# Kernel tuning notes

Measured on AMD Instinct MI355X. Metric: run time of the kernel, lower is better.

## Reference

```python
import jax, jax.numpy as jnp
import numpy as np

L, B, D, H = 128, 4, 768, 300
NT, NR = 7, 12  # ner tags, relation types
EPS = 1e-5


def _cummax(v):
    # torch: cumsum(softmax(v, -1), -1)
    return jnp.cumsum(jax.nn.softmax(v, axis=-1), axis=-1)


def _layernorm(v, g, b):
    mu = jnp.mean(v, axis=-1, keepdims=True)
    var = jnp.var(v, axis=-1, keepdims=True)
    return (v - mu) * jax.lax.rsqrt(var + EPS) * g + b


def setup_inputs() -> dict:
    key = jax.random.key(0)
    ks = jax.random.split(key, 24)
    s = lambda fan_in: 1.0 / np.sqrt(fan_in)
    u = lambda k, shape, sc: jax.random.uniform(k, shape, jnp.float32, -sc, sc)
    inp = {
        "x": jax.random.normal(ks[0], (L, B, D), jnp.float32),
        "mask": jnp.ones((L, B), jnp.float32),
        # PFN_Unit
        "W_ih": u(ks[1], (5 * H, D), s(D)), "b_ih": u(ks[2], (5 * H,), s(D)),
        "W_hh": u(ks[3], (5 * H, H), s(H)), "b_hh": u(ks[4], (5 * H,), s(H)),
        "W_tr": u(ks[5], (H, 3 * H), s(3 * H)), "b_tr": u(ks[6], (H,), s(3 * H)),
        # NERUnit
        "n_W": u(ks[7], (H, 2 * H), s(2 * H)), "n_b": u(ks[8], (H,), s(2 * H)),
        "ner_hW": u(ks[9], (H, 3 * H), s(3 * H)), "ner_hb": u(ks[10], (H,), s(3 * H)),
        "ner_g": jnp.ones((H,), jnp.float32), "ner_beta": jnp.zeros((H,), jnp.float32),
        "ner_tW": u(ks[11], (NT, H), s(H)), "ner_tb": u(ks[12], (NT,), s(H)),
        # ReUnit
        "r_W": u(ks[13], (H, 2 * H), s(2 * H)), "r_b": u(ks[14], (H,), s(2 * H)),
        "re_hW": u(ks[15], (H, 3 * H), s(3 * H)), "re_hb": u(ks[16], (H,), s(3 * H)),
        "re_g": jnp.ones((H,), jnp.float32), "re_beta": jnp.zeros((H,), jnp.float32),
        "re_tW": u(ks[17], (NR, H), s(H)), "re_tb": u(ks[18], (NR,), s(H)),
    }
    return inp


def _encoder(x, W_ih, b_ih, W_hh, b_hh, W_tr, b_tr):
    pre = jnp.einsum('lbd,gd->lbg', x, W_ih) + b_ih  # precompute input transform [L,B,5H]

    def step(carry, gx):
        h, c_in = carry
        gates = gx + h @ W_hh.T + b_hh
        c, eg_cin, rg_cin, eg_c, rg_c = jnp.split(gates, 5, axis=1)
        eg_cin, rg_cin = 1.0 - _cummax(eg_cin), _cummax(rg_cin)
        eg_c, rg_c = 1.0 - _cummax(eg_c), _cummax(rg_c)
        c = jnp.tanh(c)
        ov_c = rg_c * eg_c
        up_c, dn_c = rg_c - ov_c, eg_c - ov_c
        ov_i = rg_cin * eg_cin
        up_i, dn_i = rg_cin - ov_i, eg_cin - ov_i
        share = ov_i * c_in + ov_c * c
        c_re = up_i * c_in + up_c * c + share
        c_ner = dn_i * c_in + dn_c * c + share
        c_out = jnp.concatenate([c_re, c_ner, share], axis=-1) @ W_tr.T + b_tr
        h_out = jnp.tanh(c_out)
        return (h_out, c_out), (jnp.tanh(c_ner), jnp.tanh(c_re), jnp.tanh(share))

    h0 = jnp.zeros((x.shape[1], W_hh.shape[1]), x.dtype)
    _, (h_ner, h_re, h_share) = jax.lax.scan(step, (h0, h0), pre)
    return h_ner, h_re, h_share  # each [L,B,H]


def _pair_unit(h_task, h_share, mask, gW, gb, hW, hb, ln_g, ln_b, tW, tb, diag):
    length = h_task.shape[0]
    # global feature: tanh(Linear(cat(share, task))), max over time
    h_glob = jnp.tanh(jnp.concatenate([h_share, h_task], axis=-1) @ gW.T + gb)  # [L,B,H]
    g = jnp.max(h_glob, axis=0)  # [B,H]
    # pairwise feature [L,L,B,3H] = cat(start, end, global)
    st = jnp.broadcast_to(h_task[:, None], (length, length) + h_task.shape[1:])
    en = jnp.broadcast_to(h_task[None, :], (length, length) + h_task.shape[1:])
    gb4 = jnp.broadcast_to(g, (length, length) + g.shape)
    feat = jnp.concatenate([st, en, gb4], axis=-1)
    out = _layernorm(feat @ hW.T + hb, ln_g, ln_b)
    out = jax.nn.elu(out)  # eval mode: dropout is identity
    out = jax.nn.sigmoid(out @ tW.T + tb)  # [L,L,B,T]
    # mask
    m = mask[:, None, :] * mask[None, :, :]  # [L,L,B]
    if diag:
        m = m * jnp.triu(jnp.ones((length, length), out.dtype))[:, :, None]
    return out * m[..., None]


def reference(x, mask, W_ih, b_ih, W_hh, b_hh, W_tr, b_tr,
              n_W, n_b, ner_hW, ner_hb, ner_g, ner_beta, ner_tW, ner_tb,
              r_W, r_b, re_hW, re_hb, re_g, re_beta, re_tW, re_tb):
    h_ner, h_re, h_share = _encoder(x, W_ih, b_ih, W_hh, b_hh, W_tr, b_tr)
    ner = _pair_unit(h_ner, h_share, mask, n_W, n_b, ner_hW, ner_hb,
                     ner_g, ner_beta, ner_tW, ner_tb, diag=True)
    re = _pair_unit(h_re, h_share, mask, r_W, r_b, re_hW, re_hb,
                    re_g, re_beta, re_tW, re_tb, diag=False)
    return ner, re
```

## Files before the change

kernel.cpp:

```cpp
#include <hip/hip_runtime.h>

#define LLEN 128
#define BB 4
#define DD 768
#define HH 300
#define G5 1500
#define H3 900
#define NTT 7
#define NRR 12
#define NCHB 10
#define RPB 150
#define OPB 30

#define C_WIH  0
#define C_X    1152000
#define C_WHH2 1545216
#define C_WTR2 1995216
#define F_BIH  2265216
#define F_BTR  2266720
#define F_PRE  2267040
#define F_HG0  (F_PRE)
#define F_HG1  (F_PRE+153600)
#define F_A0   (F_PRE+307200)
#define F_E0   (F_PRE+460800)
#define F_GF0  (F_PRE+616832)
#define F_GF1  (F_PRE+618048)
#define F_HNER (F_PRE+768000)
#define F_HRE  (F_HNER+153600)
#define F_HSH  (F_HRE+153600)
#define F_A1   0
#define F_E1   153600
#define F_AUX  (F_HSH+153600)
#define AUXB   2432
#define AUX_FL 9728
#define WS_NEED_BYTES ((size_t)(F_AUX+10752)*4)

typedef unsigned short u16;
typedef unsigned int u32;

__device__ __forceinline__ float bf2f(u16 u) {
  union { u32 i; float f; } v; v.i = ((u32)u) << 16; return v.f;
}
__device__ __forceinline__ u16 f2bf(float f) {
  union { float f; u32 i; } v; v.f = f;
  u32 r = v.i + 0x7fffu + ((v.i >> 16) & 1u);
  return (u16)(r >> 16);
}
__device__ __forceinline__ float ldin(const void* p, int i, bool f32) {
  return f32 ? ((const float*)p)[i] : bf2f(((const u16*)p)[i]);
}
__device__ __forceinline__ bool is32(const void* mk) {
  return ((const u16*)mk)[0] == 0;
}
__device__ __forceinline__ float wsum(float x) {
  #pragma unroll
  for (int d = 1; d < 64; d <<= 1) x += __shfl_xor(x, d);
  return x;
}
__device__ __forceinline__ float aload(const float* p) {
  int v = __hip_atomic_load((const int*)p, __ATOMIC_RELAXED, __HIP_MEMORY_SCOPE_AGENT);
  union { int i; float f; } u; u.i = v; return u.f;
}
__device__ __forceinline__ void astore(float* p, float v) {
  union { float f; int i; } u; u.f = v;
  __hip_atomic_store((int*)p, u.i, __ATOMIC_RELAXED, __HIP_MEMORY_SCOPE_AGENT);
}
__device__ __forceinline__ void gbar(int* flag, int tid, int target) {
  __syncthreads();
  if (tid == 0) {
    __builtin_amdgcn_s_waitcnt(0);
    __hip_atomic_fetch_add(flag, 1, __ATOMIC_RELAXED, __HIP_MEMORY_SCOPE_AGENT);
    while (__hip_atomic_load(flag, __ATOMIC_RELAXED, __HIP_MEMORY_SCOPE_AGENT) < target)
      __builtin_amdgcn_s_sleep(1);
  }
  __syncthreads();
}

__global__ void k_canon(const void* xo, const void* mk, const void* Wih, const void* bih,
                        const void* Whh, const void* bhh, const void* Wtr, const void* btr,
                        float* ws) {
  bool f32 = is32(mk);
  int piece = blockIdx.y;
  int i = blockIdx.x * 256 + threadIdx.x;
  switch (piece) {
    case 0: if (!f32 && i < 1152000) ws[C_WIH + i] = ldin(Wih, i, f32); break;
    case 1: if (!f32 && i < 393216)  ws[C_X + i]   = ldin(xo, i, f32);  break;
    case 2: if (i < 225000) {
      int k2 = i / G5, out = i - k2 * G5;
      float2 v;
      v.x = ldin(Whh, out * HH + 2 * k2, f32);
      v.y = ldin(Whh, out * HH + 2 * k2 + 1, f32);
      ((float2*)(ws + C_WHH2))[i] = v;
    } break;
    case 3: if (i < 135000) {
      int k2 = i / HH, out = i - k2 * HH;
      float2 v;
      v.x = ldin(Wtr, out * H3 + 2 * k2, f32);
      v.y = ldin(Wtr, out * H3 + 2 * k2 + 1, f32);
      ((float2*)(ws + C_WTR2))[i] = v;
    } break;
    case 4: {
      if (i < 1504) ws[F_BIH + i] = (i < G5) ? ldin(bih, i, f32) + ldin(bhh, i, f32) : 0.f;
      else if (i < 1824) { int j = i - 1504; ws[F_BTR + j] = (j < HH) ? ldin(btr, j, f32) : 0.f; }
    } break;
    case 5: if (i < 1024) ((int*)(ws + F_AUX + AUX_FL))[i] = 0; break;
  }
}

__global__ void k_pre2(const void* xo, const void* Wo, const void* mk,
                       const float* cX, const float* cW, const float* biasf, float* pre) {
  bool f32 = is32(mk);
  const float* X = f32 ? (const float*)xo : cX;
  const float* W = f32 ? (const float*)Wo : cW;
  __shared__ __align__(16) float xl[8 * DD];
  int tid = threadIdx.x;
  int lb0 = (blockIdx.x >> 1) * 8;
  int half = blockIdx.x & 1;
  for (int e = tid; e < 8 * DD; e += 256) xl[e] = X[(size_t)lb0 * DD + e];
  __syncthreads();
  for (int j = half * 750 + tid; j < half * 750 + 750; j += 256) {
    const float4* w = (const float4*)(W + (size_t)j * DD);
    float acc[8] = {0.f, 0.f, 0.f, 0.f, 0.f, 0.f, 0.f, 0.f};
    #pragma unroll 2
    for (int k = 0; k < DD / 4; ++k) {
      float4 u = w[k];
      #pragma unroll
      for (int r = 0; r < 8; ++r) {
        const float4 p = *(const float4*)(xl + r * DD + k * 4);
        acc[r] += u.x * p.x + u.y * p.y + u.z * p.z + u.w * p.w;
      }
    }
    float bias = biasf[j];
    #pragma unroll
    for (int r = 0; r < 8; ++r) pre[(size_t)(lb0 + r) * G5 + j] = acc[r] + bias;
  }
}

__global__ void __launch_bounds__(512, 2) k_scan4(const float* pre, const float2* W2h, const float2* W2t,
                                                  const float* btrf, float* hner, float* hre, float* hsh,
                                                  float* aux) {
  __shared__ __align__(16) float h_l[304];
  __shared__ __align__(16) float ci_l[304];
  __shared__ __align__(16) float ga_l[1504];
  __shared__ __align__(16) float cat_l[904];
  __shared__ __align__(16) float ps[512];
  __shared__ float exv[160];
  __shared__ float pp[40];
  __shared__ float sums_l[8];
  int b = blockIdx.x / NCHB, ch = blockIdx.x % NCHB;
  int s = ch >> 1;
  int r0 = ch * RPB;
  int tid = threadIdx.x;
  float* gb   = aux + b * AUXB;
  float* cb   = gb + 1504;
  float* hb   = gb + 1808;
  float* sums = gb + 2112;
  int* flags = (int*)(aux + AUX_FL) + b * 256;
  for (int i = tid; i < 304; i += 512) { h_l[i] = 0.f; ci_l[i] = 0.f; }
  __syncthreads();
  int j = tid / RPB, r = tid - j * RPB;
  int o2 = tid % OPB, jj = tid / OPB;
  int kb = j * 100;

  float2 wh[50];
  if (tid < 450) {
    const float2* wp = W2h + (size_t)(j * 50) * G5 + (r0 + r);
    #pragma unroll
    for (int kk = 0; kk < 50; ++kk) wh[kk] = wp[(size_t)kk * G5];
  }
  float2 wt[29];
  int k2b = jj * 29;
  int k2e = (k2b + 29 < 450) ? (k2b + 29) : 450;
  int nk2 = k2e - k2b;
  if (tid < 480) {
    const float2* wp = W2t + (size_t)k2b * HH + (ch * OPB + o2);
    #pragma unroll
    for (int q = 0; q < 29; ++q) if (q < nk2) wt[q] = wp[(size_t)q * HH];
  }

  for (int t = 0; t < LLEN; ++t) {
    if (t > 0) {
      for (int i = tid; i < HH; i += 512) { h_l[i] = aload(hb + i); ci_l[i] = aload(cb + i); }
      __syncthreads();
    }
    if (tid < 450) {
      float acc = (j == 0) ? pre[((size_t)t * BB + b) * G5 + r0 + r] : 0.f;
      if (t > 0) {
        #pragma unroll
        for (int kk = 0; kk < 50; ++kk)
          acc += wh[kk].x * h_l[kb + 2 * kk] + wh[kk].y * h_l[kb + 2 * kk + 1];
      }
      ps[tid] = acc;
    }
    __syncthreads();
    if (tid < RPB) {
      float g = ps[tid] + ps[RPB + tid] + ps[2 * RPB + tid];
      if (s == 0) astore(gb + r0 + tid, tanhf(g));
      else exv[tid] = __expf(g);
    }
    __syncthreads();
    if (s > 0) {
      if (tid < 30) {
        int base = tid * 5;
        pp[tid] = ((exv[base] + exv[base+1]) + (exv[base+2] + exv[base+3])) + exv[base+4];
      }
      __syncthreads();
      if (tid == 0) {
        float run = 0.f;
        for (int i = 0; i < 30; ++i) { float tv = pp[i]; pp[i] = run; run += tv; }
        astore(sums + (ch - 2), run);
      }
      __syncthreads();
      if (tid < 30) {
        int base = tid * 5;
        float run = pp[tid];
        run += exv[base];     astore(gb + r0 + base,     run);
        run += exv[base + 1]; astore(gb + r0 + base + 1, run);
        run += exv[base + 2]; astore(gb + r0 + base + 2, run);
        run += exv[base + 3]; astore(gb + r0 + base + 3, run);
        run += exv[base + 4]; astore(gb + r0 + base + 4, run);
      }
    }
    gbar(flags + 2 * t, tid, NCHB);
    for (int i = tid; i < G5; i += 512) ga_l[i] = aload(gb + i);
    if (tid < 8) sums_l[tid] = aload(sums + tid);
    __syncthreads();
    if (tid < HH) {
      float c = ga_l[tid];
      float v[4];
      #pragma unroll
      for (int s1 = 0; s1 < 4; ++s1) {
        float raw = ga_l[(s1 + 1) * HH + tid];
        float off = (tid >= RPB) ? sums_l[2 * s1] : 0.f;
        float S = sums_l[2 * s1] + sums_l[2 * s1 + 1];
        v[s1] = (raw + off) / S;
      }
      float eg_cin = 1.f - v[0], rg_cin = v[1], eg_c = 1.f - v[2], rg_c = v[3];
      float ci = (t > 0) ? ci_l[tid] : 0.f;
      float ov_c = rg_c * eg_c;
      float up_c = rg_c - ov_c, dn_c = eg_c - ov_c;
      float ov_i = rg_cin * eg_cin;
      float up_i = rg_cin - ov_i, dn_i = eg_cin - ov_i;
      float share = ov_i * ci + ov_c * c;
      float c_re  = up_i * ci + up_c * c + share;
      float c_ner = dn_i * ci + dn_c * c + share;
      cat_l[tid] = c_re; cat_l[HH + tid] = c_ner; cat_l[2 * HH + tid] = share;
      int sb = ch * OPB;
      if (tid >= sb && tid < sb + OPB) {
        size_t ob = ((size_t)t * BB + b) * HH + tid;
        hner[ob] = tanhf(c_ner); hre[ob] = tanhf(c_re); hsh[ob] = tanhf(share);
      }
    }
    __syncthreads();
    if (tid < 480) {
      float acc = 0.f;
      #pragma unroll
      for (int q = 0; q < 29; ++q)
        if (q < nk2) acc += wt[q].x * cat_l[2 * (k2b + q)] + wt[q].y * cat_l[2 * (k2b + q) + 1];
      ps[tid] = acc;
    }
    __syncthreads();
    if (tid < OPB) {
      float co = btrf[ch * OPB + tid];
      #pragma unroll
      for (int q = 0; q < 16; ++q) co += ps[q * OPB + tid];
      astore(cb + ch * OPB + tid, co);
      astore(hb + ch * OPB + tid, tanhf(co));
    }
    gbar(flags + 2 * t + 1, tid, NCHB);
  }
}

__global__ void k_glob3(const float* hsh, const float* hner, const float* hre,
                        const void* nW, const void* nb, const void* rW, const void* rb,
                        const void* mk, float* hg0, float* hg1) {
  bool f32 = is32(mk);
  int task = blockIdx.x >> 7;
  int lb0 = (blockIdx.x & 127) * 4;
  const float* tsk = task ? hre : hner;
  const void* gWo = task ? rW : nW;
  const void* gbo = task ? rb : nb;
  float* hg = task ? hg1 : hg0;
  __shared__ __align__(16) float catl[2400];
  int tid = threadIdx.x;
  for (int e = tid; e < 2400; e += 320) {
    int rr = e / 600, c = e - rr * 600;
    catl[e] = (c < HH) ? hsh[(size_t)(lb0 + rr) * HH + c] : tsk[(size_t)(lb0 + rr) * HH + (c - HH)];
  }
  __syncthreads();
  if (tid < HH) {
    float bias = ldin(gbo, tid, f32);
    float acc[4] = {bias, bias, bias, bias};
    if (f32) {
      const float4* row = (const float4*)((const float*)gWo + (size_t)tid * 600);
      #pragma unroll 2
      for (int k = 0; k < 150; ++k) {
        float4 u = row[k];
        #pragma unroll
        for (int rr = 0; rr < 4; ++rr) {
          const float4 cv = *(const float4*)(catl + rr * 600 + 4 * k);
          acc[rr] += u.x * cv.x + u.y * cv.y + u.z * cv.z + u.w * cv.w;
        }
      }
    } else {
      for (int k = 0; k < 600; ++k) {
        float w = ldin(gWo, tid * 600 + k, f32);
        #pragma unroll
        for (int rr = 0; rr < 4; ++rr) acc[rr] += w * catl[rr * 600 + k];
      }
    }
    #pragma unroll
    for (int rr = 0; rr < 4; ++rr) hg[(size_t)(lb0 + rr) * HH + tid] = tanhf(acc[rr]);
  }
}

__global__ void k_feat2(const float* hner, const float* hre,
                        const void* nhW, const void* nhb, const void* rhW, const void* rhb,
                        const void* mk, float* A0, float* E0, float* A1, float* E1) {
  bool f32 = is32(mk);
  int task = blockIdx.x >> 7;
  int lb0 = (blockIdx.x & 127) * 4;
  const float* tsk = task ? hre : hner;
  const void* hWo = task ? rhW : nhW;
  const void* hbo = task ? rhb : nhb;
  float* A = task ? A1 : A0;
  float* E = task ? E1 : E0;
  __shared__ __align__(16) float tl[1200];
  int tid = threadIdx.x;
  for (int e = tid; e < 1200; e += 320) {
    int rr = e / 300, c = e - rr * 300;
    tl[e] = tsk[(size_t)(lb0 + rr) * HH + c];
  }
  __syncthreads();
  if (tid < HH) {
    float bias = ldin(hbo, tid, f32);
    float a[4] = {bias, bias, bias, bias};
    float ev[4] = {0.f, 0.f, 0.f, 0.f};
    if (f32) {
      const float4* r1 = (const float4*)((const float*)hWo + (size_t)tid * H3);
      const float4* r2 = (const float4*)((const float*)hWo + (size_t)tid * H3 + HH);
      #pragma unroll 2
      for (int k = 0; k < 75; ++k) {
        float4 u = r1[k], w2 = r2[k];
        #pragma unroll
        for (int rr = 0; rr < 4; ++rr) {
          const float4 tv = *(const float4*)(tl + rr * 300 + 4 * k);
          a[rr]  += u.x * tv.x + u.y * tv.y + u.z * tv.z + u.w * tv.w;
          ev[rr] += w2.x * tv.x + w2.y * tv.y + w2.z * tv.z + w2.w * tv.w;
        }
      }
    } else {
      for (int k = 0; k < HH; ++k) {
        float w1 = ldin(hWo, tid * H3 + k, f32);
        float w2 = ldin(hWo, tid * H3 + HH + k, f32);
        #pragma unroll
        for (int rr = 0; rr < 4; ++rr) {
          a[rr] += w1 * tl[rr * 300 + k];
          ev[rr] += w2 * tl[rr * 300 + k];
        }
      }
    }
    #pragma unroll
    for (int rr = 0; rr < 4; ++rr) {
      A[(size_t)(lb0 + rr) * HH + tid] = a[rr];
      E[(size_t)(lb0 + rr) * HH + tid] = ev[rr];
    }
  }
}

__global__ void k_gmf(const float* hg0, const float* hg1, const void* nhW, const void* rhW,
                      const void* mk, float* Gf0, float* Gf1) {
  bool f32 = is32(mk);
  int task = blockIdx.x >> 2, b = blockIdx.x & 3;
  const float* hg = task ? hg1 : hg0;
  const void* hWo = task ? rhW : nhW;
  float* Gf = task ? Gf1 : Gf0;
  __shared__ __align__(16) float gl[304];
  int tid = threadIdx.x;
  if (tid < HH) {
    float m = -1e30f;
    for (int l = 0; l < LLEN; ++l) m = fmaxf(m, hg[((size_t)l * BB + b) * HH + tid]);
    gl[tid] = m;
  }
  __syncthreads();
  if (tid < HH) {
    float acc = 0.f;
    if (f32) {
      const float4* row = (const float4*)((const float*)hWo + (size_t)tid * H3 + 600);
      #pragma unroll 5
      for (int k = 0; k < 75; ++k) {
        float4 u = row[k];
        const float4 gv = *(const float4*)(gl + 4 * k);
        acc += u.x * gv.x + u.y * gv.y + u.z * gv.z + u.w * gv.w;
      }
    } else {
      for (int k = 0; k < HH; ++k) acc += gl[k] * ldin(hWo, tid * H3 + 600 + k, f32);
    }
    Gf[b * HH + tid] = acc;
  }
}

__global__ void __launch_bounds__(256) k_pair6(const float* A0, const float* E0, const float* Gf0,
                                               const void* lg0, const void* lb0_, const void* tW0, const void* tb0,
                                               const float* A1, const float* E1, const float* Gf1,
                                               const void* lg1, const void* lb1_, const void* tW1, const void* tb1,
                                               const void* mk, void* outv) {
  __shared__ float lg_l[304], lb_l[304], tb_l[16];
  __shared__ float tw_l[3616];
  bool f32 = is32(mk);
  int tau = blockIdx.x >> 12;
  int bid = blockIdx.x & 4095;
  const float* A  = tau ? A1 : A0;
  const float* E  = tau ? E1 : E0;
  const float* Gf = tau ? Gf1 : Gf0;
  const void* lgo = tau ? lg1 : lg0;
  const void* lbo = tau ? lb1_ : lb0_;
  const void* tWo = tau ? tW1 : tW0;
  const void* tbo = tau ? tb1 : tb0;
  int T = tau ? NRR : NTT;
  int diag = tau ? 0 : 1;
  int Toff = tau ? 458752 : 0;
  int tid = threadIdx.x;
  for (int i2 = tid; i2 < HH; i2 += 256) { lg_l[i2] = ldin(lgo, i2, f32); lb_l[i2] = ldin(lbo, i2, f32); }
  for (int i2 = tid; i2 < T * HH; i2 += 256) tw_l[i2] = ldin(tWo, i2, f32);
  if (tid < T) tb_l[tid] = ldin(tbo, tid, f32);
  __syncthreads();
  int i = bid >> 5;
  int j0 = (bid & 31) << 2;
  int b = tid >> 6, ln = tid & 63;
  const float* ar = A  + (size_t)(i * BB + b) * HH;
  const float* gr = Gf + (size_t)b * HH;
  bool ok4 = ln < 44;
  float a0 = ar[ln]       + gr[ln];
  float a1 = ar[64 + ln]  + gr[64 + ln];
  float a2 = ar[128 + ln] + gr[128 + ln];
  float a3 = ar[192 + ln] + gr[192 + ln];
  float a4 = ok4 ? (ar[256 + ln] + gr[256 + ln]) : 0.f;
  float mi = ldin(mk, i * BB + b, f32);
  for (int dj = 0; dj < 4; ++dj) {
    int jx = j0 + dj;
    const float* er = E + (size_t)(jx * BB + b) * HH;
    float u0 = a0 + er[ln];
    float u1 = a1 + er[64 + ln];
    float u2 = a2 + er[128 + ln];
    float u3 = a3 + er[192 + ln];
    float u4 = ok4 ? (a4 + er[256 + ln]) : 0.f;
    float s1 = ((u0 + u1) + (u2 + u3)) + u4;
    float s2 = ((u0 * u0 + u1 * u1) + (u2 * u2 + u3 * u3)) + u4 * u4;
    #pragma unroll
    for (int d = 1; d < 64; d <<= 1) { s1 += __shfl_xor(s1, d); s2 += __shfl_xor(s2, d); }
    float mean = s1 * (1.f / 300.f);
    float var = s2 * (1.f / 300.f) - mean * mean;
    float rstd = rsqrtf(var + 1e-5f);
    {
      float y;
      y = (u0 - mean) * rstd * lg_l[ln]       + lb_l[ln];       u0 = (y > 0.f) ? y : __expf(y) - 1.f;
      y = (u1 - mean) * rstd * lg_l[64 + ln]  + lb_l[64 + ln];  u1 = (y > 0.f) ? y : __expf(y) - 1.f;
      y = (u2 - mean) * rstd * lg_l[128 + ln] + lb_l[128 + ln]; u2 = (y > 0.f) ? y : __expf(y) - 1.f;
      y = (u3 - mean) * rstd * lg_l[192 + ln] + lb_l[192 + ln]; u3 = (y > 0.f) ? y : __expf(y) - 1.f;
      if (ok4) {
        y = (u4 - mean) * rstd * lg_l[256 + ln] + lb_l[256 + ln];
        u4 = (y > 0.f) ? y : __expf(y) - 1.f;
      }
    }
    float m = mi * ldin(mk, jx * BB + b, f32);
    if (diag && jx < i) m = 0.f;
    size_t obase = (size_t)Toff + ((size_t)(i * LLEN + jx) * BB + b) * T;
    float mine = 0.f;
    for (int t = 0; t < T; ++t) {
      const float* twr = tw_l + t * HH;
      float s = u0 * twr[ln] + u1 * twr[64 + ln] + u2 * twr[128 + ln] + u3 * twr[192 + ln];
      if (ok4) s += u4 * twr[256 + ln];
      s = wsum(s);
      s += tb_l[t];
      float o = m / (1.f + __expf(-s));
      mine = (ln == t) ? o : mine;
    }
    if (ln < T) {
      if (f32) ((float*)outv)[obase + ln] = mine;
      else ((u16*)outv)[obase + ln] = f2bf(mine);
    }
  }
}

__global__ void k_sent(const void* mk, const void* xo, void* outv, int hostcode) {
  __shared__ int bad;
  if (threadIdx.x == 0) bad = 0;
  __syncthreads();
  bool f32 = is32(mk);
  for (int i = threadIdx.x; i < 4096; i += 256) {
    float v = ldin(xo, i, f32);
    if (!(v == v) || fabsf(v) > 1e6f) bad = 1;
  }
  __syncthreads();
  if (threadIdx.x == 0) {
    float code = (float)hostcode;
    if (bad) code = fmaxf(code, 88.f);
    if (code > 0.f) {
      if (f32) ((float*)outv)[0] = code;
      else ((u16*)outv)[0] = f2bf(code);
    }
  }
}

extern "C" void kernel_launch(void* const* d_in, const int* in_sizes, int n_in,
                              void* d_out, int out_size, void* d_ws, size_t ws_size,
                              hipStream_t stream) {
  const void* x    = d_in[0];
  const void* mask = d_in[1];
  const void* Wih  = d_in[2];
  const void* bih  = d_in[3];
  const void* Whh  = d_in[4];
  const void* bhh  = d_in[5];
  const void* Wtr  = d_in[6];
  const void* btr  = d_in[7];
  const void* nW   = d_in[8];
  const void* nb   = d_in[9];
  const void* nhW  = d_in[10];
  const void* nhb  = d_in[11];
  const void* ng   = d_in[12];
  const void* nbe  = d_in[13];
  const void* ntW  = d_in[14];
  const void* ntb  = d_in[15];
  const void* rW   = d_in[16];
  const void* rb   = d_in[17];
  const void* rhW  = d_in[18];
  const void* rhb  = d_in[19];
  const void* rg   = d_in[20];
  const void* rbe  = d_in[21];
  const void* rtW  = d_in[22];
  const void* rtb  = d_in[23];
  float* ws = (float*)d_ws;

  static const int exp_sz[24] = {393216, 512, 1152000, 1500, 450000, 1500, 270000, 300,
                                 180000, 300, 270000, 300, 300, 300, 2100, 7,
                                 180000, 300, 270000, 300, 300, 300, 3600, 12};
  int hostcode = 0;
  if (n_in != 24) hostcode = 890;
  else {
    for (int ii = 0; ii < 24; ++ii)
      if (in_sizes[ii] != exp_sz[ii]) { hostcode = 900 + ii; break; }
  }
  if (hostcode == 0 && out_size != 1245184) hostcode = 880;
  if (hostcode == 0 && ws_size < WS_NEED_BYTES) hostcode = 1099;

  dim3 gc(4500, 6);
  k_canon<<<gc, 256, 0, stream>>>(x, mask, Wih, bih, Whh, bhh, Wtr, btr, ws);
  k_pre2<<<128, 256, 0, stream>>>(x, Wih, mask, ws + C_X, ws + C_WIH, ws + F_BIH, ws + F_PRE);
  k_scan4<<<40, 512, 0, stream>>>(ws + F_PRE, (const float2*)(ws + C_WHH2), (const float2*)(ws + C_WTR2),
                                  ws + F_BTR, ws + F_HNER, ws + F_HRE, ws + F_HSH, ws + F_AUX);
  k_glob3<<<256, 320, 0, stream>>>(ws + F_HSH, ws + F_HNER, ws + F_HRE,
                                   nW, nb, rW, rb, mask, ws + F_HG0, ws + F_HG1);
  k_feat2<<<256, 320, 0, stream>>>(ws + F_HNER, ws + F_HRE, nhW, nhb, rhW, rhb, mask,
                                   ws + F_A0, ws + F_E0, ws + F_A1, ws + F_E1);
  k_gmf<<<8, 320, 0, stream>>>(ws + F_HG0, ws + F_HG1, nhW, rhW, mask, ws + F_GF0, ws + F_GF1);
  k_pair6<<<8192, 256, 0, stream>>>(ws + F_A0, ws + F_E0, ws + F_GF0, ng, nbe, ntW, ntb,
                                    ws + F_A1, ws + F_E1, ws + F_GF1, rg, rbe, rtW, rtb,
                                    mask, d_out);
  k_sent<<<1, 256, 0, stream>>>(mask, x, d_out, hostcode);
}
```

Measured before the change: 1.544 ms.

## Drop weight transposes, fuse glob/feat kernels, widen pair tiles, warp-scan prefix

The scan kernel now reads W_hh and W_tr straight from the original inputs in row-major form instead of from pre-transposed workspace copies, so the canon kernel no longer transposes them. Canon is split into a bf16-only conversion kernel that exits early for fp32 inputs plus a small kernel for biases and flag clearing. The glob and feat kernels are merged into one launch, and the pair kernel gives each block 8 columns instead of 4, halving its grid. The serial 30-element prefix sum in the scan is replaced by a shuffle-based wave scan. Per-thread weight loads in the scan become strided in a different pattern, which may change how coalesced they are.

```diff
diff --git a/kernel.cpp b/kernel.cpp
--- a/kernel.cpp
+++ b/kernel.cpp
@@ -14,8 +14,6 @@
 
 #define C_WIH  0
 #define C_X    1152000
-#define C_WHH2 1545216
-#define C_WTR2 1995216
 #define F_BIH  2265216
 #define F_BTR  2266720
 #define F_PRE  2267040
@@ -76,35 +74,20 @@
   __syncthreads();
 }
 
-__global__ void k_canon(const void* xo, const void* mk, const void* Wih, const void* bih,
-                        const void* Whh, const void* bhh, const void* Wtr, const void* btr,
-                        float* ws) {
-  bool f32 = is32(mk);
+__global__ void k_canon2(const void* xo, const void* mk, const void* Wih, float* ws) {
+  if (is32(mk)) return;
   int piece = blockIdx.y;
   int i = blockIdx.x * 256 + threadIdx.x;
-  switch (piece) {
-    case 0: if (!f32 && i < 1152000) ws[C_WIH + i] = ldin(Wih, i, f32); break;
-    case 1: if (!f32 && i < 393216)  ws[C_X + i]   = ldin(xo, i, f32);  break;
-    case 2: if (i < 225000) {
-      int k2 = i / G5, out = i - k2 * G5;
-      float2 v;
-      v.x = ldin(Whh, out * HH + 2 * k2, f32);
-      v.y = ldin(Whh, out * HH + 2 * k2 + 1, f32);
-      ((float2*)(ws + C_WHH2))[i] = v;
-    } break;
-    case 3: if (i < 135000) {
-      int k2 = i / HH, out = i - k2 * HH;
-      float2 v;
-      v.x = ldin(Wtr, out * H3 + 2 * k2, f32);
-      v.y = ldin(Wtr, out * H3 + 2 * k2 + 1, f32);
-      ((float2*)(ws + C_WTR2))[i] = v;
-    } break;
-    case 4: {
-      if (i < 1504) ws[F_BIH + i] = (i < G5) ? ldin(bih, i, f32) + ldin(bhh, i, f32) : 0.f;
-      else if (i < 1824) { int j = i - 1504; ws[F_BTR + j] = (j < HH) ? ldin(btr, j, f32) : 0.f; }
-    } break;
-    case 5: if (i < 1024) ((int*)(ws + F_AUX + AUX_FL))[i] = 0; break;
-  }
+  if (piece == 0) { if (i < 1152000) ws[C_WIH + i] = bf2f(((const u16*)Wih)[i]); }
+  else            { if (i < 393216)  ws[C_X + i]   = bf2f(((const u16*)xo)[i]); }
+}
+
+__global__ void k_misc(const void* bih, const void* bhh, const void* btr, const void* mk, float* ws) {
+  bool f32 = is32(mk);
+  int i = blockIdx.x * 256 + threadIdx.x;
+  if (i < 1504) ws[F_BIH + i] = (i < G5) ? ldin(bih, i, f32) + ldin(bhh, i, f32) : 0.f;
+  else if (i < 1824) { int j = i - 1504; ws[F_BTR + j] = (j < HH) ? ldin(btr, j, f32) : 0.f; }
+  else if (i >= 2048 && i < 3072) ((int*)(ws + F_AUX + AUX_FL))[i - 2048] = 0;
 }
 
 __global__ void k_pre2(const void* xo, const void* Wo, const void* mk,
@@ -136,9 +119,9 @@
   }
 }
 
-__global__ void __launch_bounds__(512, 2) k_scan4(const float* pre, const float2* W2h, const float2* W2t,
-                                                  const float* btrf, float* hner, float* hre, float* hsh,
-                                                  float* aux) {
+__global__ void __launch_bounds__(512, 2) k_scan5(const float* pre, const void* Whh, const void* Wtr,
+                                                  const void* mk, const float* btrf,
+                                                  float* hner, float* hre, float* hsh, float* aux) {
   __shared__ __align__(16) float h_l[304];
   __shared__ __align__(16) float ci_l[304];
   __shared__ __align__(16) float ga_l[1504];
@@ -147,6 +130,7 @@
   __shared__ float exv[160];
   __shared__ float pp[40];
   __shared__ float sums_l[8];
+  bool f32 = is32(mk);
   int b = blockIdx.x / NCHB, ch = blockIdx.x % NCHB;
   int s = ch >> 1;
   int r0 = ch * RPB;
@@ -164,18 +148,31 @@
 
   float2 wh[50];
   if (tid < 450) {
-    const float2* wp = W2h + (size_t)(j * 50) * G5 + (r0 + r);
-    #pragma unroll
-    for (int kk = 0; kk < 50; ++kk) wh[kk] = wp[(size_t)kk * G5];
+    if (f32) {
+      const float2* wp = (const float2*)((const float*)Whh + (size_t)(r0 + r) * HH + kb);
+      #pragma unroll
+      for (int kk = 0; kk < 50; ++kk) wh[kk] = wp[kk];
+    } else {
+      const u16* wp = (const u16*)Whh + (size_t)(r0 + r) * HH + kb;
+      #pragma unroll
+      for (int kk = 0; kk < 50; ++kk) { wh[kk].x = bf2f(wp[2 * kk]); wh[kk].y = bf2f(wp[2 * kk + 1]); }
+    }
   }
   float2 wt[29];
   int k2b = jj * 29;
   int k2e = (k2b + 29 < 450) ? (k2b + 29) : 450;
   int nk2 = k2e - k2b;
   if (tid < 480) {
-    const float2* wp = W2t + (size_t)k2b * HH + (ch * OPB + o2);
-    #pragma unroll
-    for (int q = 0; q < 29; ++q) if (q < nk2) wt[q] = wp[(size_t)q * HH];
+    int out = ch * OPB + o2;
+    if (f32) {
+      const float2* wp = (const float2*)((const float*)Wtr + (size_t)out * H3 + 2 * k2b);
+      #pragma unroll
+      for (int q = 0; q < 29; ++q) if (q < nk2) wt[q] = wp[q];
+    } else {
+      const u16* wp = (const u16*)Wtr + (size_t)out * H3 + 2 * k2b;
+      #pragma unroll
+      for (int q = 0; q < 29; ++q) if (q < nk2) { wt[q].x = bf2f(wp[2 * q]); wt[q].y = bf2f(wp[2 * q + 1]); }
+    }
   }
 
   for (int t = 0; t < LLEN; ++t) {
@@ -205,10 +202,13 @@
         pp[tid] = ((exv[base] + exv[base+1]) + (exv[base+2] + exv[base+3])) + exv[base+4];
       }
       __syncthreads();
-      if (tid == 0) {
-        float run = 0.f;
-        for (int i = 0; i < 30; ++i) { float tv = pp[i]; pp[i] = run; run += tv; }
-        astore(sums + (ch - 2), run);
+      if (tid < 64) {
+        float v = (tid < 30) ? pp[tid] : 0.f;
+        float inc = v;
+        #pragma unroll
+        for (int d = 1; d < 32; d <<= 1) { float t2 = __shfl_up(inc, d); if (tid >= d) inc += t2; }
+        if (tid < 30) pp[tid] = inc - v;
+        if (tid == 29) astore(sums + (ch - 2), inc);
       }
       __syncthreads();
       if (tid < 30) {
@@ -271,99 +271,95 @@
   }
 }
 
-__global__ void k_glob3(const float* hsh, const float* hner, const float* hre,
-                        const void* nW, const void* nb, const void* rW, const void* rb,
-                        const void* mk, float* hg0, float* hg1) {
-  bool f32 = is32(mk);
-  int task = blockIdx.x >> 7;
+__global__ void k_globfeat(const float* hsh, const float* hner, const float* hre,
+                           const void* nW, const void* nb, const void* rW, const void* rb,
+                           const void* nhW, const void* nhb, const void* rhW, const void* rhb,
+                           const void* mk, float* hg0, float* hg1,
+                           float* A0, float* E0, float* A1, float* E1) {
+  bool f32 = is32(mk);
+  int sel = blockIdx.x >> 8;
+  int task = (blockIdx.x >> 7) & 1;
   int lb0 = (blockIdx.x & 127) * 4;
   const float* tsk = task ? hre : hner;
-  const void* gWo = task ? rW : nW;
-  const void* gbo = task ? rb : nb;
-  float* hg = task ? hg1 : hg0;
-  __shared__ __align__(16) float catl[2400];
   int tid = threadIdx.x;
-  for (int e = tid; e < 2400; e += 320) {
-    int rr = e / 600, c = e - rr * 600;
-    catl[e] = (c < HH) ? hsh[(size_t)(lb0 + rr) * HH + c] : tsk[(size_t)(lb0 + rr) * HH + (c - HH)];
-  }
-  __syncthreads();
-  if (tid < HH) {
-    float bias = ldin(gbo, tid, f32);
-    float acc[4] = {bias, bias, bias, bias};
-    if (f32) {
-      const float4* row = (const float4*)((const float*)gWo + (size_t)tid * 600);
-      #pragma unroll 2
-      for (int k = 0; k < 150; ++k) {
-        float4 u = row[k];
-        #pragma unroll
-        for (int rr = 0; rr < 4; ++rr) {
-          const float4 cv = *(const float4*)(catl + rr * 600 + 4 * k);
-          acc[rr] += u.x * cv.x + u.y * cv.y + u.z * cv.z + u.w * cv.w;
+  if (sel == 0) {
+    const void* gWo = task ? rW : nW;
+    const void* gbo = task ? rb : nb;
+    float* hg = task ? hg1 : hg0;
+    __shared__ __align__(16) float catl[2400];
+    for (int e = tid; e < 2400; e += 320) {
+      int rr = e / 600, c = e - rr * 600;
+      catl[e] = (c < HH) ? hsh[(size_t)(lb0 + rr) * HH + c] : tsk[(size_t)(lb0 + rr) * HH + (c - HH)];
+    }
+    __syncthreads();
+    if (tid < HH) {
+      float bias = ldin(gbo, tid, f32);
+      float acc[4] = {bias, bias, bias, bias};
+      if (f32) {
+        const float4* row = (const float4*)((const float*)gWo + (size_t)tid * 600);
+        #pragma unroll 2
+        for (int k = 0; k < 150; ++k) {
+          float4 u = row[k];
+          #pragma unroll
+          for (int rr = 0; rr < 4; ++rr) {
+            const float4 cv = *(const float4*)(catl + rr * 600 + 4 * k);
+            acc[rr] += u.x * cv.x + u.y * cv.y + u.z * cv.z + u.w * cv.w;
+          }
         }
-      }
-    } else {
-      for (int k = 0; k < 600; ++k) {
-        float w = ldin(gWo, tid * 600 + k, f32);
-        #pragma unroll
-        for (int rr = 0; rr < 4; ++rr) acc[rr] += w * catl[rr * 600 + k];
-      }
-    }
-    #pragma unroll
-    for (int rr = 0; rr < 4; ++rr) hg[(size_t)(lb0 + rr) * HH + tid] = tanhf(acc[rr]);
-  }
-}
-
-__global__ void k_feat2(const float* hner, const float* hre,
-                        const void* nhW, const void* nhb, const void* rhW, const void* rhb,
-                        const void* mk, float* A0, float* E0, float* A1, float* E1) {
-  bool f32 = is32(mk);
-  int task = blockIdx.x >> 7;
-  int lb0 = (blockIdx.x & 127) * 4;
-  const float* tsk = task ? hre : hner;
-  const void* hWo = task ? rhW : nhW;
-  const void* hbo = task ? rhb : nhb;
-  float* A = task ? A1 : A0;
-  float* E = task ? E1 : E0;
-  __shared__ __align__(16) float tl[1200];
-  int tid = threadIdx.x;
-  for (int e = tid; e < 1200; e += 320) {
-    int rr = e / 300, c = e - rr * 300;
-    tl[e] = tsk[(size_t)(lb0 + rr) * HH + c];
-  }
-  __syncthreads();
-  if (tid < HH) {
-    float bias = ldin(hbo, tid, f32);
-    float a[4] = {bias, bias, bias, bias};
-    float ev[4] = {0.f, 0.f, 0.f, 0.f};
-    if (f32) {
-      const float4* r1 = (const float4*)((const float*)hWo + (size_t)tid * H3);
-      const float4* r2 = (const float4*)((const float*)hWo + (size_t)tid * H3 + HH);
-      #pragma unroll 2
-      for (int k = 0; k < 75; ++k) {
-        float4 u = r1[k], w2 = r2[k];
-        #pragma unroll
-        for (int rr = 0; rr < 4; ++rr) {
-          const float4 tv = *(const float4*)(tl + rr * 300 + 4 * k);
-          a[rr]  += u.x * tv.x + u.y * tv.y + u.z * tv.z + u.w * tv.w;
-          ev[rr] += w2.x * tv.x + w2.y * tv.y + w2.z * tv.z + w2.w * tv.w;
+      } else {
+        for (int k = 0; k < 600; ++k) {
+          float w = ldin(gWo, tid * 600 + k, f32);
+          #pragma unroll
+          for (int rr = 0; rr < 4; ++rr) acc[rr] += w * catl[rr * 600 + k];
         }
       }
-    } else {
-      for (int k = 0; k < HH; ++k) {
-        float w1 = ldin(hWo, tid * H3 + k, f32);
-        float w2 = ldin(hWo, tid * H3 + HH + k, f32);
-        #pragma unroll
-        for (int rr = 0; rr < 4; ++rr) {
-          a[rr] += w1 * tl[rr * 300 + k];
-          ev[rr] += w2 * tl[rr * 300 + k];
+      #pragma unroll
+      for (int rr = 0; rr < 4; ++rr) hg[(size_t)(lb0 + rr) * HH + tid] = tanhf(acc[rr]);
+    }
+  } else {
+    const void* hWo = task ? rhW : nhW;
+    const void* hbo = task ? rhb : nhb;
+    float* A = task ? A1 : A0;
+    float* E = task ? E1 : E0;
+    __shared__ __align__(16) float tl[1200];
+    for (int e = tid; e < 1200; e += 320) {
+      int rr = e / 300, c = e - rr * 300;
+      tl[e] = tsk[(size_t)(lb0 + rr) * HH + c];
+    }
+    __syncthreads();
+    if (tid < HH) {
+      float bias = ldin(hbo, tid, f32);
+      float a[4] = {bias, bias, bias, bias};
+      float ev[4] = {0.f, 0.f, 0.f, 0.f};
+      if (f32) {
+        const float4* r1 = (const float4*)((const float*)hWo + (size_t)tid * H3);
+        const float4* r2 = (const float4*)((const float*)hWo + (size_t)tid * H3 + HH);
+        #pragma unroll 2
+        for (int k = 0; k < 75; ++k) {
+          float4 u = r1[k], w2 = r2[k];
+          #pragma unroll
+          for (int rr = 0; rr < 4; ++rr) {
+            const float4 tv = *(const float4*)(tl + rr * 300 + 4 * k);
+            a[rr]  += u.x * tv.x + u.y * tv.y + u.z * tv.z + u.w * tv.w;
+            ev[rr] += w2.x * tv.x + w2.y * tv.y + w2.z * tv.z + w2.w * tv.w;
+          }
         }
-      }
-    }
-    #pragma unroll
-    for (int rr = 0; rr < 4; ++rr) {
-      A[(size_t)(lb0 + rr) * HH + tid] = a[rr];
-      E[(size_t)(lb0 + rr) * HH + tid] = ev[rr];
+      } else {
+        for (int k = 0; k < HH; ++k) {
+          float w1 = ldin(hWo, tid * H3 + k, f32);
+          float w2 = ldin(hWo, tid * H3 + HH + k, f32);
+          #pragma unroll
+          for (int rr = 0; rr < 4; ++rr) {
+            a[rr] += w1 * tl[rr * 300 + k];
+            ev[rr] += w2 * tl[rr * 300 + k];
+          }
+        }
+      }
+      #pragma unroll
+      for (int rr = 0; rr < 4; ++rr) {
+        A[(size_t)(lb0 + rr) * HH + tid] = a[rr];
+        E[(size_t)(lb0 + rr) * HH + tid] = ev[rr];
+      }
     }
   }
 }
@@ -400,7 +396,7 @@
   }
 }
 
-__global__ void __launch_bounds__(256) k_pair6(const float* A0, const float* E0, const float* Gf0,
+__global__ void __launch_bounds__(256) k_pair7(const float* A0, const float* E0, const float* Gf0,
                                                const void* lg0, const void* lb0_, const void* tW0, const void* tb0,
                                                const float* A1, const float* E1, const float* Gf1,
                                                const void* lg1, const void* lb1_, const void* tW1, const void* tb1,
@@ -408,8 +404,8 @@
   __shared__ float lg_l[304], lb_l[304], tb_l[16];
   __shared__ float tw_l[3616];
   bool f32 = is32(mk);
-  int tau = blockIdx.x >> 12;
-  int bid = blockIdx.x & 4095;
+  int tau = blockIdx.x >> 11;
+  int bid = blockIdx.x & 2047;
   const float* A  = tau ? A1 : A0;
   const float* E  = tau ? E1 : E0;
   const float* Gf = tau ? Gf1 : Gf0;
@@ -425,8 +421,8 @@
   for (int i2 = tid; i2 < T * HH; i2 += 256) tw_l[i2] = ldin(tWo, i2, f32);
   if (tid < T) tb_l[tid] = ldin(tbo, tid, f32);
   __syncthreads();
-  int i = bid >> 5;
-  int j0 = (bid & 31) << 2;
+  int i = bid >> 4;
+  int j0 = (bid & 15) << 3;
   int b = tid >> 6, ln = tid & 63;
   const float* ar = A  + (size_t)(i * BB + b) * HH;
   const float* gr = Gf + (size_t)b * HH;
@@ -437,7 +433,7 @@
   float a3 = ar[192 + ln] + gr[192 + ln];
   float a4 = ok4 ? (ar[256 + ln] + gr[256 + ln]) : 0.f;
   float mi = ldin(mk, i * BB + b, f32);
-  for (int dj = 0; dj < 4; ++dj) {
+  for (int dj = 0; dj < 8; ++dj) {
     int jx = j0 + dj;
     const float* er = E + (size_t)(jx * BB + b) * HH;
     float u0 = a0 + er[ln];
@@ -544,17 +540,18 @@
   if (hostcode == 0 && out_size != 1245184) hostcode = 880;
   if (hostcode == 0 && ws_size < WS_NEED_BYTES) hostcode = 1099;
 
-  dim3 gc(4500, 6);
-  k_canon<<<gc, 256, 0, stream>>>(x, mask, Wih, bih, Whh, bhh, Wtr, btr, ws);
+  dim3 gc(4500, 2);
+  k_canon2<<<gc, 256, 0, stream>>>(x, mask, Wih, ws);
+  k_misc<<<12, 256, 0, stream>>>(bih, bhh, btr, mask, ws);
   k_pre2<<<128, 256, 0, stream>>>(x, Wih, mask, ws + C_X, ws + C_WIH, ws + F_BIH, ws + F_PRE);
-  k_scan4<<<40, 512, 0, stream>>>(ws + F_PRE, (const float2*)(ws + C_WHH2), (const float2*)(ws + C_WTR2),
-                                  ws + F_BTR, ws + F_HNER, ws + F_HRE, ws + F_HSH, ws + F_AUX);
-  k_glob3<<<256, 320, 0, stream>>>(ws + F_HSH, ws + F_HNER, ws + F_HRE,
-                                   nW, nb, rW, rb, mask, ws + F_HG0, ws + F_HG1);
-  k_feat2<<<256, 320, 0, stream>>>(ws + F_HNER, ws + F_HRE, nhW, nhb, rhW, rhb, mask,
-                                   ws + F_A0, ws + F_E0, ws + F_A1, ws + F_E1);
+  k_scan5<<<40, 512, 0, stream>>>(ws + F_PRE, Whh, Wtr, mask, ws + F_BTR,
+                                  ws + F_HNER, ws + F_HRE, ws + F_HSH, ws + F_AUX);
+  k_globfeat<<<512, 320, 0, stream>>>(ws + F_HSH, ws + F_HNER, ws + F_HRE,
+                                      nW, nb, rW, rb, nhW, nhb, rhW, rhb, mask,
+                                      ws + F_HG0, ws + F_HG1,
+                                      ws + F_A0, ws + F_E0, ws + F_A1, ws + F_E1);
   k_gmf<<<8, 320, 0, stream>>>(ws + F_HG0, ws + F_HG1, nhW, rhW, mask, ws + F_GF0, ws + F_GF1);
-  k_pair6<<<8192, 256, 0, stream>>>(ws + F_A0, ws + F_E0, ws + F_GF0, ng, nbe, ntW, ntb,
+  k_pair7<<<4096, 256, 0, stream>>>(ws + F_A0, ws + F_E0, ws + F_GF0, ng, nbe, ntW, ntb,
                                     ws + F_A1, ws + F_E1, ws + F_GF1, rg, rbe, rtW, rtb,
                                     mask, d_out);
   k_sent<<<1, 256, 0, stream>>>(mask, x, d_out, hostcode);
```

New measurement: 1.602 ms. 1.04x slower.
